# Kernel tuning notes

Measured on AMD Instinct MI355X. Metric: run time of the kernel, lower is better.

Reference implementation:

```python
import jax, jax.numpy as jnp
import numpy as np

NUM_PROB_BINS = 15
NUM_CLASSES = 8
NEIGHBORHOOD_WIDTH = 3
NUM_NEIGHBOR_CLASSES = NEIGHBORHOOD_WIDTH ** 2  # 9
B, H, W = 16, 512, 512


def _bin_index(x, nbins):
    # Uniform bins on [0, 1]: bin_idx = floor(x * nbins), last bin closed at 1.0.
    idx = jnp.floor(x * nbins).astype(jnp.int32)
    return jnp.clip(idx, 0, nbins - 1)


def setup_inputs() -> dict:
    key = jax.random.key(0)
    k1, k2 = jax.random.split(key)
    logits = jax.random.normal(k1, (B, NUM_CLASSES, H, W), dtype=jnp.float32)
    # Precomputed calibration frequency table: [num_classes, num_neighbor_bins, num_prob_bins]
    val_freqs = jax.random.uniform(k2, (NUM_CLASSES, NUM_NEIGHBOR_CLASSES, NUM_PROB_BINS), dtype=jnp.float32)
    return {"logits": logits, "val_freqs": val_freqs}


def reference(logits, val_freqs):
    probs = jax.nn.softmax(logits, axis=1)  # [B, C, H, W]
    kw = NEIGHBORHOOD_WIDTH
    # agg_neighbors_preds (soft, class_wise): mean prob over kw x kw spatial neighborhood.
    neigh_mean = jax.lax.reduce_window(
        probs, 0.0, jax.lax.add,
        window_dimensions=(1, 1, kw, kw),
        window_strides=(1, 1, 1, 1),
        padding='SAME',
    ) / float(kw * kw)
    loc_bin = _bin_index(neigh_mean, NUM_NEIGHBOR_CLASSES)  # [B,C,H,W] int32 in [0,9)
    prob_bin = _bin_index(probs, NUM_PROB_BINS)             # [B,C,H,W] int32 in [0,15)
    # The nested class/neighbor-bin loops + masked assignment collapse to one fused gather:
    cls_idx = jnp.arange(NUM_CLASSES, dtype=jnp.int32)[None, :, None, None]
    calibrated = val_freqs[cls_idx, loc_bin, prob_bin]       # [B,C,H,W]
    # normalize=True branch
    s = jnp.sum(calibrated, axis=1, keepdims=True)
    s = jnp.where(s == 0, jnp.ones_like(s), s)
    return calibrated / s
```

## Files before the change

### kernel.cpp

```cpp
#include <hip/hip_runtime.h>
#include <math.h>

constexpr int NPB = 15;
constexpr int NC  = 8;
constexpr int NNB = 9;
constexpr int Bn  = 16;
constexpr int Hc  = 512;
constexpr int Wc  = 512;

constexpr int TX = 32, TY = 8;
constexpr int HX = TX + 2;
constexpr int HY = TY + 2;

__global__ __launch_bounds__(256)
void nectar_kernel(const float* __restrict__ logits,
                   const float* __restrict__ vf,
                   float* __restrict__ out)
{
    __shared__ float sP[NC][HY][HX];
    __shared__ float sVF[NC * NNB * NPB];

    const int tid = threadIdx.x;
    const int x0  = blockIdx.x * TX;
    const int y0  = blockIdx.y * TY;
    const int b   = blockIdx.z;

    for (int i = tid; i < NC * NNB * NPB; i += 256) sVF[i] = vf[i];

    const size_t plane = (size_t)Hc * Wc;
    const float* src = logits + (size_t)b * NC * plane;

    for (int i = tid; i < HX * HY; i += 256) {
        const int ly = i / HX;
        const int lx = i - ly * HX;
        const int gy = y0 + ly - 1;
        const int gx = x0 + lx - 1;
        if ((unsigned)gy < (unsigned)Hc && (unsigned)gx < (unsigned)Wc) {
            const float* p = src + (size_t)gy * Wc + gx;
            float v[NC];
            #pragma unroll
            for (int c = 0; c < NC; c++) v[c] = p[(size_t)c * plane];
            float m = v[0];
            #pragma unroll
            for (int c = 1; c < NC; c++) m = fmaxf(m, v[c]);
            float e[NC];
            float S = 0.0f;
            #pragma unroll
            for (int c = 0; c < NC; c++) {
                float d = v[c] - m;
                e[c] = (float)exp((double)d);
                S = S + e[c];
            }
            #pragma unroll
            for (int c = 0; c < NC; c++) sP[c][ly][lx] = e[c] / S;
        } else {
            #pragma unroll
            for (int c = 0; c < NC; c++) sP[c][ly][lx] = 0.0f;
        }
    }
    __syncthreads();

    const int lx = tid & (TX - 1);
    const int ly = tid >> 5;
    const int gx = x0 + lx;
    const int gy = y0 + ly;

    float cal[NC];
    float s = 0.0f;
    #pragma unroll
    for (int c = 0; c < NC; c++) {
        float acc = 0.0f;
        #pragma unroll
        for (int dy = 0; dy < 3; dy++) {
            #pragma unroll
            for (int dx = 0; dx < 3; dx++) {
                acc = acc + sP[c][ly + dy][lx + dx];
            }
        }
        float nm = acc / 9.0f;
        int lb = (int)floorf(nm * 9.0f);
        lb = lb < 0 ? 0 : (lb > NNB - 1 ? NNB - 1 : lb);
        float pcv = sP[c][ly + 1][lx + 1];
        int pb = (int)floorf(pcv * 15.0f);
        pb = pb < 0 ? 0 : (pb > NPB - 1 ? NPB - 1 : pb);
        cal[c] = sVF[(c * NNB + lb) * NPB + pb];
        s = s + cal[c];
    }
    if (s == 0.0f) s = 1.0f;

    float* dst = out + (size_t)b * NC * plane + (size_t)gy * Wc + gx;
    #pragma unroll
    for (int c = 0; c < NC; c++) dst[(size_t)c * plane] = cal[c] / s;
}

extern "C" void kernel_launch(void* const* d_in, const int* in_sizes, int n_in,
                              void* d_out, int out_size, void* d_ws, size_t ws_size,
                              hipStream_t stream) {
    const float* logits = (const float*)d_in[0];
    const float* vf     = (const float*)d_in[1];
    float* out          = (float*)d_out;

    dim3 grid(Wc / TX, Hc / TY, Bn);
    dim3 block(256);
    nectar_kernel<<<grid, block, 0, stream>>>(logits, vf, out);
}
```

Baseline: 260.8 us.

## Compute two output rows per thread and replace libm double exp with custom routine

The tile height doubles from 8 to 16 rows, so each thread now produces two vertically adjacent outputs and reuses the shared-memory rows the two 3x3 windows have in common. This reduces halo recomputation of the softmax per output pixel and lowers the number of blocks. The double-precision libm exp is replaced by an inlined double polynomial with range reduction, meant to be cheaper while staying accurate. There is a small risk of bin-boundary mismatches if the custom exp differs in the last bits.

Measured after the change: 255.8 us. Within noise of the previous version (-1.9%).

```diff
diff --git a/kernel.cpp b/kernel.cpp
--- a/kernel.cpp
+++ b/kernel.cpp
@@ -8,11 +8,38 @@
 constexpr int Hc  = 512;
 constexpr int Wc  = 512;
 
-constexpr int TX = 32, TY = 8;
+constexpr int TX = 32, TY = 16;
 constexpr int HX = TX + 2;
 constexpr int HY = TY + 2;
+constexpr int NT = 256;
 
-__global__ __launch_bounds__(256)
+__device__ __forceinline__ float exp_f32_cr(float df) {
+    const double d  = (double)df;
+    const double TWO_LOG2E  = 2.8853900817779268;
+    const double NLN2_2_HI  = -0.34657359018456190824;
+    const double NLN2_2_LO  = -9.5410746463529385e-11;
+    double t  = d * TWO_LOG2E;
+    double kd = rint(t);
+    int    k  = (int)kd;
+    double r  = fma(kd, NLN2_2_HI, d);
+    r = fma(kd, NLN2_2_LO, r);
+    double p = 2.7557319223985893e-6;
+    p = fma(p, r, 2.4801587301587302e-5);
+    p = fma(p, r, 1.9841269841269841e-4);
+    p = fma(p, r, 1.3888888888888889e-3);
+    p = fma(p, r, 8.3333333333333333e-3);
+    p = fma(p, r, 4.1666666666666664e-2);
+    p = fma(p, r, 1.6666666666666666e-1);
+    p = fma(p, r, 0.5);
+    p = fma(p, r, 1.0);
+    p = fma(p, r, 1.0);
+    double sc = (k & 1) ? 1.4142135623730951 : 1.0;
+    double v  = p * sc;
+    long long bits = __double_as_longlong(v) + ((long long)(k >> 1) << 52);
+    return (float)__longlong_as_double(bits);
+}
+
+__global__ __launch_bounds__(NT)
 void nectar_kernel(const float* __restrict__ logits,
                    const float* __restrict__ vf,
                    float* __restrict__ out)
@@ -25,12 +52,12 @@
     const int y0  = blockIdx.y * TY;
     const int b   = blockIdx.z;
 
-    for (int i = tid; i < NC * NNB * NPB; i += 256) sVF[i] = vf[i];
+    for (int i = tid; i < NC * NNB * NPB; i += NT) sVF[i] = vf[i];
 
     const size_t plane = (size_t)Hc * Wc;
     const float* src = logits + (size_t)b * NC * plane;
 
-    for (int i = tid; i < HX * HY; i += 256) {
+    for (int i = tid; i < HX * HY; i += NT) {
         const int ly = i / HX;
         const int lx = i - ly * HX;
         const int gy = y0 + ly - 1;
@@ -43,16 +70,14 @@
             float m = v[0];
             #pragma unroll
             for (int c = 1; c < NC; c++) m = fmaxf(m, v[c]);
-            float e[NC];
             float S = 0.0f;
             #pragma unroll
             for (int c = 0; c < NC; c++) {
-                float d = v[c] - m;
-                e[c] = (float)exp((double)d);
-                S = S + e[c];
+                v[c] = exp_f32_cr(v[c] - m);
+                S = S + v[c];
             }
             #pragma unroll
-            for (int c = 0; c < NC; c++) sP[c][ly][lx] = e[c] / S;
+            for (int c = 0; c < NC; c++) sP[c][ly][lx] = v[c] / S;
         } else {
             #pragma unroll
             for (int c = 0; c < NC; c++) sP[c][ly][lx] = 0.0f;
@@ -60,37 +85,47 @@
     }
     __syncthreads();
 
-    const int lx = tid & (TX - 1);
-    const int ly = tid >> 5;
-    const int gx = x0 + lx;
-    const int gy = y0 + ly;
+    const int lx  = tid & (TX - 1);
+    const int lyg = tid >> 5;
+    const int oy0 = lyg * 2;
+    const int gx  = x0 + lx;
+    const int gy0 = y0 + oy0;
 
-    float cal[NC];
-    float s = 0.0f;
+    float cal0[NC], cal1[NC];
+    float s0 = 0.0f, s1 = 0.0f;
     #pragma unroll
     for (int c = 0; c < NC; c++) {
-        float acc = 0.0f;
-        #pragma unroll
-        for (int dy = 0; dy < 3; dy++) {
-            #pragma unroll
-            for (int dx = 0; dx < 3; dx++) {
-                acc = acc + sP[c][ly + dy][lx + dx];
-            }
-        }
-        float nm = acc / 9.0f;
-        int lb = (int)floorf(nm * 9.0f);
-        lb = lb < 0 ? 0 : (lb > NNB - 1 ? NNB - 1 : lb);
-        float pcv = sP[c][ly + 1][lx + 1];
-        int pb = (int)floorf(pcv * 15.0f);
-        pb = pb < 0 ? 0 : (pb > NPB - 1 ? NPB - 1 : pb);
-        cal[c] = sVF[(c * NNB + lb) * NPB + pb];
-        s = s + cal[c];
+        float r0a = sP[c][oy0 + 0][lx], r0b = sP[c][oy0 + 0][lx + 1], r0c = sP[c][oy0 + 0][lx + 2];
+        float r1a = sP[c][oy0 + 1][lx], r1b = sP[c][oy0 + 1][lx + 1], r1c = sP[c][oy0 + 1][lx + 2];
+        float r2a = sP[c][oy0 + 2][lx], r2b = sP[c][oy0 + 2][lx + 1], r2c = sP[c][oy0 + 2][lx + 2];
+        float r3a = sP[c][oy0 + 3][lx], r3b = sP[c][oy0 + 3][lx + 1], r3c = sP[c][oy0 + 3][lx + 2];
+        float a0 = ((((((((r0a + r0b) + r0c) + r1a) + r1b) + r1c) + r2a) + r2b) + r2c);
+        float a1 = ((((((((r1a + r1b) + r1c) + r2a) + r2b) + r2c) + r3a) + r3b) + r3c);
+
+        float nm0 = a0 / 9.0f;
+        float nm1 = a1 / 9.0f;
+        int lb0 = (int)floorf(nm0 * 9.0f);
+        int lb1 = (int)floorf(nm1 * 9.0f);
+        lb0 = lb0 < 0 ? 0 : (lb0 > NNB - 1 ? NNB - 1 : lb0);
+        lb1 = lb1 < 0 ? 0 : (lb1 > NNB - 1 ? NNB - 1 : lb1);
+        int pb0 = (int)floorf(r1b * 15.0f);
+        int pb1 = (int)floorf(r2b * 15.0f);
+        pb0 = pb0 < 0 ? 0 : (pb0 > NPB - 1 ? NPB - 1 : pb0);
+        pb1 = pb1 < 0 ? 0 : (pb1 > NPB - 1 ? NPB - 1 : pb1);
+        cal0[c] = sVF[(c * NNB + lb0) * NPB + pb0];
+        cal1[c] = sVF[(c * NNB + lb1) * NPB + pb1];
+        s0 = s0 + cal0[c];
+        s1 = s1 + cal1[c];
     }
-    if (s == 0.0f) s = 1.0f;
+    if (s0 == 0.0f) s0 = 1.0f;
+    if (s1 == 0.0f) s1 = 1.0f;
 
-    float* dst = out + (size_t)b * NC * plane + (size_t)gy * Wc + gx;
+    float* dst = out + (size_t)b * NC * plane + (size_t)gy0 * Wc + gx;
     #pragma unroll
-    for (int c = 0; c < NC; c++) dst[(size_t)c * plane] = cal[c] / s;
+    for (int c = 0; c < NC; c++) {
+        dst[(size_t)c * plane]      = cal0[c] / s0;
+        dst[(size_t)c * plane + Wc] = cal1[c] / s1;
+    }
 }
 
 extern "C" void kernel_launch(void* const* d_in, const int* in_sizes, int n_in,
@@ -101,6 +136,6 @@
     float* out          = (float*)d_out;
 
     dim3 grid(Wc / TX, Hc / TY, Bn);
-    dim3 block(256);
+    dim3 block(NT);
     nectar_kernel<<<grid, block, 0, stream>>>(logits, vf, out);
 }
```
